# Optimization experiments

Measured on AMD Instinct MI355X. Metric: run time of the kernel, lower is better.

## Reference

```python
import jax, jax.numpy as jnp
import numpy as np

E = 512   # embed_size == hidden_size (required: step-0 'embed' is the init output of size hidden)
H = 512
A = 512   # attention dim
V = 20000
P = 196
B = 128
T = 24


def setup_inputs() -> dict:
    key = jax.random.key(0)
    ks = jax.random.split(key, 20)
    s = 0.02
    return {
        "features": jax.random.normal(ks[0], (B, P, E), jnp.float32),
        "captions": jax.random.randint(ks[1], (B, T), 0, V),
        "emb": jax.random.normal(ks[2], (V, E), jnp.float32) * s,
        "W_init_h": jax.random.normal(ks[3], (E, H), jnp.float32) * s,
        "b_init_h": jnp.zeros((H,), jnp.float32),
        "W_init_o": jax.random.normal(ks[4], (E, H), jnp.float32) * s,
        "b_init_o": jnp.zeros((H,), jnp.float32),
        "Wf": jax.random.normal(ks[5], (E, A), jnp.float32) * s,
        "bf": jnp.zeros((A,), jnp.float32),
        "Wh": jax.random.normal(ks[6], (H, A), jnp.float32) * s,
        "bh": jnp.zeros((A,), jnp.float32),
        "v_att": jax.random.normal(ks[7], (A,), jnp.float32) * s,
        "W_ih": jax.random.normal(ks[8], (3 * H, 2 * E), jnp.float32) * s,
        "W_hh": jax.random.normal(ks[9], (3 * H, H), jnp.float32) * s,
        "b_ih": jnp.zeros((3 * H,), jnp.float32),
        "b_hh": jnp.zeros((3 * H,), jnp.float32),
        "W_out": jax.random.normal(ks[10], (V, H), jnp.float32) * s,
        "b_out": jnp.zeros((V,), jnp.float32),
    }


def reference(features, emb, W_init_h, b_init_h, W_init_o, b_init_o,
              Wf, bf, Wh, bh, v_att, W_ih, W_hh, b_ih, b_hh,
              W_out, b_out, captions):
    # init_hidden_state
    avg = features.mean(axis=1)                          # [B,E]
    hidden0 = jnp.tanh(avg @ W_init_h + b_init_h)        # [B,H]
    output0 = jnp.tanh(avg @ W_init_o + b_init_o)        # [B,H]

    emb_caps = emb[captions]                             # [B,T,E]
    # teacher forcing: step 0 uses init output, step i>0 uses embeddings[:, i-1]
    embed_seq = jnp.concatenate([output0[:, None, :], emb_caps[:, :-1, :]], axis=1)
    xs = embed_seq.transpose(1, 0, 2)                    # [T,B,E]

    feat_proj = features @ Wf + bf                       # [B,P,A] (precompute attn key proj)

    def step(h, x_emb):
        # additive attention over pixels
        score = jnp.tanh(feat_proj + (h @ Wh + bh)[:, None, :]) @ v_att   # [B,P]
        alpha = jax.nn.softmax(score, axis=1)
        ctx = jnp.einsum('bp,bpe->be', alpha, features)                   # [B,E]
        x = jnp.concatenate([x_emb, ctx], axis=1)                         # [B,2E]
        # single-step GRU (PyTorch gate order r,z,n)
        gi = x @ W_ih.T + b_ih
        gh = h @ W_hh.T + b_hh
        gi_r, gi_z, gi_n = jnp.split(gi, 3, axis=1)
        gh_r, gh_z, gh_n = jnp.split(gh, 3, axis=1)
        r = jax.nn.sigmoid(gi_r + gh_r)
        z = jax.nn.sigmoid(gi_z + gh_z)
        n = jnp.tanh(gi_n + r * gh_n)
        h_new = (1.0 - z) * n + z * h
        pred = h_new @ W_out.T + b_out                                    # [B,V]
        return h_new, pred

    _, preds = jax.lax.scan(step, hidden0, xs)           # preds: [T,B,V]
    return preds.transpose(1, 0, 2)                      # [B,T,V]
```

## Files before the change

### kernel.cpp

```cpp
#include <hip/hip_runtime.h>

#define Bb 128
#define Tt 24
#define Ee 512
#define Hh 512
#define Aa 512
#define Vv 20000
#define Pp 196
#define TV (Tt*Vv)
#define NBLK 512
#define NTHR 256
#define GT (NBLK*NTHR)

typedef __attribute__((ext_vector_type(8))) short bfrag;
typedef __attribute__((ext_vector_type(4))) float f4;
typedef __attribute__((ext_vector_type(4))) unsigned short us4;
typedef __attribute__((ext_vector_type(2))) unsigned long long u64x2;

#define MFMA16(a,b,c) __builtin_amdgcn_mfma_f32_16x16x32_bf16(a,b,c,0,0,0)

__device__ __forceinline__ unsigned short f2bf(float f){
  unsigned int x = __builtin_bit_cast(unsigned int, f);
  x += 0x7fffu + ((x >> 16) & 1u);
  return (unsigned short)(x >> 16);
}
__device__ __forceinline__ float bfu2f(unsigned short u){
  unsigned int x = ((unsigned int)u) << 16;
  return __builtin_bit_cast(float, x);
}
#define LOG2E 1.442695041f
__device__ __forceinline__ float fexp2(float x){ return __builtin_amdgcn_exp2f(x); }
__device__ __forceinline__ float frcp (float x){ return __builtin_amdgcn_rcpf(x); }
__device__ __forceinline__ float tanh_f(float x){ return 1.0f - 2.0f*frcp(1.0f + fexp2((2.0f*LOG2E)*x)); }
__device__ __forceinline__ float sigm_f(float x){ return frcp(1.0f + fexp2(-LOG2E*x)); }

__device__ __forceinline__ unsigned long long scld8(const void* p){
  return __hip_atomic_load((const unsigned long long*)p, __ATOMIC_RELAXED, __HIP_MEMORY_SCOPE_AGENT);
}
__device__ __forceinline__ unsigned scld4(const unsigned* p){
  return __hip_atomic_load(p, __ATOMIC_RELAXED, __HIP_MEMORY_SCOPE_AGENT);
}
__device__ __forceinline__ bfrag scld_frag(const unsigned short* p){
  u64x2 v;
  v.x = scld8(p);
  v.y = scld8(p + 4);
  return __builtin_bit_cast(bfrag, v);
}
__device__ __forceinline__ void scst4(unsigned* p, unsigned v){
  __hip_atomic_store(p, v, __ATOMIC_RELAXED, __HIP_MEMORY_SCOPE_AGENT);
}
__device__ __forceinline__ void scstf(float* p, float v){
  __hip_atomic_store(p, v, __ATOMIC_RELAXED, __HIP_MEMORY_SCOPE_AGENT);
}

__device__ __forceinline__ void set_flag(unsigned* line, unsigned v){
  asm volatile("s_waitcnt vmcnt(0)" ::: "memory");
  __syncthreads();
  if(threadIdx.x == 0) scst4(line, v);
}
__device__ __forceinline__ void poll_flags(const unsigned* base, int n, unsigned tgt){
  int tid = threadIdx.x;
  for(;;){
    int ok = (tid < n) ? (scld4(base + tid*16) >= tgt) : 1;
    if(__syncthreads_count(ok) == NTHR) break;
    __builtin_amdgcn_s_sleep(2);
  }
  asm volatile("" ::: "memory");
}

__device__ __forceinline__ void gbar2(unsigned* sync, unsigned phase){
  __syncthreads();
  int tid = threadIdx.x, blk = blockIdx.x;
  if(tid == 0)
    (void)__hip_atomic_fetch_add(sync + (blk & 31)*16, 1u,
                                 __ATOMIC_RELEASE, __HIP_MEMORY_SCOPE_AGENT);
  if(blk == 0){
    for(;;){
      int ok = (tid < 32) ? (scld4(sync + tid*16) >= phase*16u) : 1;
      if(__syncthreads_count(ok) == NTHR) break;
      __builtin_amdgcn_s_sleep(2);
    }
    if(tid == 0) scst4(sync + 32*16, phase);
  }
  if(tid == 0){
    while(scld4(sync + 32*16) < phase) __builtin_amdgcn_s_sleep(2);
    (void)__hip_atomic_load(sync + 32*16, __ATOMIC_ACQUIRE, __HIP_MEMORY_SCOPE_AGENT);
  }
  __syncthreads();
}

__global__ void k_zero(unsigned* s){
  int i = blockIdx.x*256 + threadIdx.x;
  s[i] = 0u;
}

__device__ __forceinline__ void cast_loop(const float* __restrict__ s,
                                          unsigned short* __restrict__ d,
                                          int n4, int gtid){
  for(int i = gtid; i < n4; i += GT){
    float4 v = ((const float4*)s)[i];
    us4 o; o[0]=f2bf(v.x); o[1]=f2bf(v.y); o[2]=f2bf(v.z); o[3]=f2bf(v.w);
    ((us4*)d)[i] = o;
  }
}
__device__ __forceinline__ void tr_tile(const float* __restrict__ S,
                                        unsigned short* __restrict__ D,
                                        int it, int jt, int tid, float (*T)[33]){
  int er = tid>>3, c4 = (tid&7)*4;
  float4 v = *(const float4*)(S + (size_t)(jt*32+er)*512 + it*32 + c4);
  T[er][c4+0]=v.x; T[er][c4+1]=v.y; T[er][c4+2]=v.z; T[er][c4+3]=v.w;
  __syncthreads();
  us4 o;
  o[0]=f2bf(T[c4+0][er]); o[1]=f2bf(T[c4+1][er]);
  o[2]=f2bf(T[c4+2][er]); o[3]=f2bf(T[c4+3][er]);
  *(us4*)(D + (size_t)(it*32+er)*512 + jt*32 + c4) = o;
  __syncthreads();
}


__device__ void attention_task(int b, const float* __restrict__ hpr,
                               const unsigned short* __restrict__ fpb,
                               const unsigned short* __restrict__ featsB,
                               const float* __restrict__ vatt,
                               unsigned short* __restrict__ ctxb, char* SM)
{
  float* hp  = (float*)SM;
  float* vp  = hp + 512;
  float* sc  = vp + 512;
  float* red = sc + 200;
  int tid = threadIdx.x;
  {
    unsigned long long q = scld8(hpr + (size_t)b*Aa + tid*2);
    float2 hv = __builtin_bit_cast(float2, q);
    float2 vv = *(const float2*)(vatt + tid*2);
    int a0 = tid*2, a1 = tid*2+1;
    hp[((a0&31)<<4)+(a0>>5)] = hv.x;
    hp[((a1&31)<<4)+(a1>>5)] = hv.y;
    vp[((a0&31)<<4)+(a0>>5)] = vv.x;
    vp[((a1&31)<<4)+(a1>>5)] = vv.y;
  }
  __syncthreads();
  int grp = tid >> 4, gl = tid & 15;
  for(int pass=0; pass<13; pass++){
    int p = pass*16 + grp;
    float acc = 0.0f;
    if(p < Pp){
      const unsigned short* fr = fpb + ((size_t)b*Pp + p)*Aa + gl*32;
      #pragma unroll
      for(int j=0;j<32;j+=8){
        bfrag fv = *(const bfrag*)(fr + j);
        #pragma unroll
        for(int q=0;q<8;q++){
          int idx = ((j+q)<<4) + gl;
          float x = bfu2f((unsigned short)fv[q]) + hp[idx];
          acc += tanh_f(x) * vp[idx];
        }
      }
    }
    acc += __shfl_xor(acc, 1, 64);
    acc += __shfl_xor(acc, 2, 64);
    acc += __shfl_xor(acc, 4, 64);
    acc += __shfl_xor(acc, 8, 64);
    if(p < Pp && gl == 0) sc[p] = acc;
  }
  __syncthreads();
  if(tid < 64){
    float m = -1e30f;
    for(int i=0;i<4;i++){ int p = tid + i*64; if(p < Pp) m = fmaxf(m, sc[p]); }
    for(int off=1; off<64; off<<=1) m = fmaxf(m, __shfl_xor(m, off, 64));
    float s = 0.0f;
    for(int i=0;i<4;i++){ int p = tid + i*64; if(p < Pp) s += fexp2((sc[p]-m)*LOG2E); }
    for(int off=1; off<64; off<<=1) s += __shfl_xor(s, off, 64);
    if(tid == 0){ red[0] = m; red[1] = frcp(s); }
  }
  __syncthreads();
  float mx = red[0], rS = red[1];
  float al_t = 0.0f;
  if(tid < Pp) al_t = fexp2((sc[tid]-mx)*LOG2E) * rS;
  __syncthreads();
  if(tid < Pp) sc[tid] = al_t;
  __syncthreads();
  float c0 = 0.f, c1 = 0.f;
  const unsigned int* fb = (const unsigned int*)(featsB + (size_t)b*Pp*Ee);
  for(int p=0;p<Pp;p++){
    float al = sc[p];
    unsigned int u = fb[(size_t)p*256 + tid];
    unsigned int lo = (u & 0xffffu) << 16, hi = u & 0xffff0000u;
    c0 += al * __builtin_bit_cast(float, lo);
    c1 += al * __builtin_bit_cast(float, hi);
  }
  unsigned int cw = ((unsigned int)f2bf(c1) << 16) | (unsigned int)f2bf(c0);
  scst4((unsigned*)ctxb + (size_t)b*256 + tid, cw);
}

__device__ void gates_phaseA(int g, const unsigned short* __restrict__ hbs,
                             const unsigned short* __restrict__ aemb,
                             const unsigned short* __restrict__ WihB,
                             const unsigned short* __restrict__ WhhB,
                             f4 (&agh)[2][3], f4 (&agi)[2][3])
{
  int tid = threadIdx.x;
  int w = tid>>6, l = tid&63, l16 = l&15, lk = l>>4;
  int hs = g*16 + l16, m0 = w*32;
  #pragma unroll
  for(int mi=0;mi<2;mi++) for(int q=0;q<3;q++){ agh[mi][q]=(f4)(0.f); agi[mi][q]=(f4)(0.f); }
  bfrag ah0 = scld_frag(hbs + (size_t)(m0+l16)*Hh + lk*8);
  bfrag ah1 = scld_frag(hbs + (size_t)(m0+16+l16)*Hh + lk*8);
  for(int k0=0;k0<512;k0+=32){
    int koff = k0 + lk*8;
    bfrag nh0 = ah0, nh1 = ah1;
    if(k0+32 < 512){
      nh0 = scld_frag(hbs + (size_t)(m0+l16)*Hh + koff + 32);
      nh1 = scld_frag(hbs + (size_t)(m0+16+l16)*Hh + koff + 32);
    }
    bfrag ae0 = *(const bfrag*)(aemb + (size_t)(m0+l16)*Ee + koff);
    bfrag ae1 = *(const bfrag*)(aemb + (size_t)(m0+16+l16)*Ee + koff);
    #pragma unroll
    for(int q=0;q<3;q++){
      int j = q*512 + hs;
      bfrag bh_ = *(const bfrag*)(WhhB + (size_t)j*512  + koff);
      bfrag be  = *(const bfrag*)(WihB + (size_t)j*1024 + koff);
      agh[0][q] = MFMA16(ah0, bh_, agh[0][q]);
      agh[1][q] = MFMA16(ah1, bh_, agh[1][q]);
      agi[0][q] = MFMA16(ae0, be,  agi[0][q]);
      agi[1][q] = MFMA16(ae1, be,  agi[1][q]);
    }
    ah0 = nh0; ah1 = nh1;
  }
}

__device__ void gates_phaseB(int g, const unsigned short* __restrict__ ctxb,
                             const unsigned short* __restrict__ WihB,
                             const float* __restrict__ bih, const float* __restrict__ bhh,
                             const float* __restrict__ hf_cur, float* __restrict__ hf_nxt,
                             unsigned short* __restrict__ hb_nxt,
                             f4 (&agh)[2][3], f4 (&agi)[2][3], char* SM)
{
  unsigned short (*HB)[16] = (unsigned short(*)[16])SM;
  int tid = threadIdx.x;
  int w = tid>>6, l = tid&63, l16 = l&15, lk = l>>4;
  int hs = g*16 + l16, m0 = w*32;
  bfrag ac0 = scld_frag(ctxb + (size_t)(m0+l16)*Ee + lk*8);
  bfrag ac1 = scld_frag(ctxb + (size_t)(m0+16+l16)*Ee + lk*8);
  for(int k0=0;k0<512;k0+=32){
    int koff = k0 + lk*8;
    bfrag nc0 = ac0, nc1 = ac1;
    if(k0+32 < 512){
      nc0 = scld_frag(ctxb + (size_t)(m0+l16)*Ee + koff + 32);
      nc1 = scld_frag(ctxb + (size_t)(m0+16+l16)*Ee + koff + 32);
    }
    #pragma unroll
    for(int q=0;q<3;q++){
      int j = q*512 + hs;
      bfrag bc = *(const bfrag*)(WihB + (size_t)j*1024 + 512 + koff);
      agi[0][q] = MFMA16(ac0, bc, agi[0][q]);
      agi[1][q] = MFMA16(ac1, bc, agi[1][q]);
    }
    ac0 = nc0; ac1 = nc1;
  }
  float bir = bih[hs],      bhr = bhh[hs];
  float biz = bih[512+hs],  bhz = bhh[512+hs];
  float bin = bih[1024+hs], bhn = bhh[1024+hs];
  #pragma unroll
  for(int mi=0;mi<2;mi++){
    #pragma unroll
    for(int i=0;i<4;i++){
      int b = m0 + mi*16 + lk*4 + i;
      float r = sigm_f(agi[mi][0][i] + bir + agh[mi][0][i] + bhr);
      float z = sigm_f(agi[mi][1][i] + biz + agh[mi][1][i] + bhz);
      float n = tanh_f(agi[mi][2][i] + bin + r*(agh[mi][2][i] + bhn));
      float ho = hf_cur[(size_t)b*Hh + hs];
      float hn = (1.0f - z)*n + z*ho;
      hf_nxt[(size_t)b*Hh + hs] = hn;
      HB[b][l16] = f2bf(hn);
    }
  }
  __syncthreads();
  #pragma unroll
  for(int j2=0;j2<4;j2++){
    int wix = tid + j2*256;
    int bb = wix >> 3, pr = wix & 7;
    unsigned u = (unsigned)HB[bb][pr*2] | ((unsigned)HB[bb][pr*2+1] << 16);
    scst4((unsigned*)(hb_nxt + (size_t)bb*Hh + g*16) + pr, u);
  }
}

__device__ void hproj_task(int g, const unsigned short* __restrict__ hbsrc,
                           const unsigned short* __restrict__ WhT,
                           const float* __restrict__ bhv, float* __restrict__ hpr)
{
  int tid = threadIdx.x;
  int w = tid>>6, l = tid&63, l16 = l&15, lk = l>>4;
  int m0 = w*32;
  int a = g*16 + l16;
  f4 acc[2]; acc[0]=(f4)(0.0f); acc[1]=(f4)(0.0f);
  bfrag af0 = scld_frag(hbsrc + (size_t)(m0+l16)*Hh + lk*8);
  bfrag af1 = scld_frag(hbsrc + (size_t)(m0+16+l16)*Hh + lk*8);
  for(int k0=0;k0<512;k0+=32){
    int koff = k0 + lk*8;
    bfrag n0 = af0, n1 = af1;
    if(k0+32 < 512){
      n0 = scld_frag(hbsrc + (size_t)(m0+l16)*Hh + koff + 32);
      n1 = scld_frag(hbsrc + (size_t)(m0+16+l16)*Hh + koff + 32);
    }
    bfrag bq = *(const bfrag*)(WhT + (size_t)a*Hh + koff);
    acc[0] = MFMA16(af0, bq, acc[0]);
    acc[1] = MFMA16(af1, bq, acc[1]);
    af0 = n0; af1 = n1;
  }
  float bias = bhv[a];
  #pragma unroll
  for(int mi=0;mi<2;mi++)
    #pragma unroll
    for(int i=0;i<4;i++){
      int b = m0 + mi*16 + lk*4 + i;
      scstf(hpr + (size_t)b*Aa + a, acc[mi][i] + bias);
    }
}

__device__ void pred_task(int pt, int tw, const unsigned short* __restrict__ hb_cur,
                          const unsigned short* __restrict__ WoutB,
                          const float* __restrict__ bout, float* __restrict__ out,
                          char* SM)
{
  int tid = threadIdx.x;
  int vchunk = pt >> 1, mbase = (pt & 1)*64;
  for(int j=0;j<32;j++){
    int u = tid + j*256;
    int row = u >> 7, c8 = u & 127;
    unsigned long long q = scld8(hb_cur + (size_t)(mbase+row)*Hh + c8*4);
    int bo = (row<<10) + (c8<<3);
    bo ^= (row&7)<<4;
    *(unsigned long long*)(SM + bo) = q;
  }
  __syncthreads();
  int w = tid>>6, l = tid&63, l16 = l&15, lk = l>>4;
  int nb = vchunk*128 + w*32;
  f4 acc[4][2];
  #pragma unroll
  for(int mi=0;mi<4;mi++) for(int ni=0;ni<2;ni++) acc[mi][ni] = (f4)(0.0f);
  for(int k0=0;k0<512;k0+=32){
    int koff = k0 + lk*8;
    bfrag af[4], bq[2];
    #pragma unroll
    for(int mi=0;mi<4;mi++){
      int row = mi*16 + l16;
      int bo = (row<<10) + (koff<<1);
      bo ^= (row&7)<<4;
      af[mi] = *(const bfrag*)(SM + bo);
    }
    #pragma unroll
    for(int ni=0;ni<2;ni++){
      int v = nb + ni*16 + l16; if(v > Vv-1) v = Vv-1;
      bq[ni] = *(const bfrag*)(WoutB + (size_t)v*Hh + koff);
    }
    #pragma unroll
    for(int mi=0;mi<4;mi++)
      #pragma unroll
      for(int ni=0;ni<2;ni++)
        acc[mi][ni] = MFMA16(af[mi], bq[ni], acc[mi][ni]);
  }
  #pragma unroll
  for(int ni=0;ni<2;ni++){
    int v = nb + ni*16 + l16;
    if(v < Vv){
      float bias = bout[v];
      #pragma unroll
      for(int mi=0;mi<4;mi++){
        #pragma unroll
        for(int i=0;i<4;i++){
          int br = mbase + mi*16 + lk*4 + i;
          __builtin_nontemporal_store(acc[mi][ni][i] + bias,
              out + (size_t)br*TV + (size_t)tw*Vv + v);
        }
      }
    }
  }
  __syncthreads();
}

__global__ __launch_bounds__(NTHR, 2) void k_all(
    const float* feats, const int* caps, const float* emb,
    const float* Winh, const float* binh, const float* Wino, const float* bino,
    const float* Wf, const float* bfv, const float* Wh, const float* bhv,
    const float* vatt, const float* Wih, const float* Whh,
    const float* bih, const float* bhh, const float* Wout, const float* bout,
    float* out,
    float* hfR, unsigned short* hbR, float* hpr,
    unsigned short* ctxR, unsigned short* avgB, unsigned short* eseq,
    unsigned short* WfT, unsigned short* WhT,
    unsigned short* WinhT, unsigned short* WinoT,
    unsigned short* WihB, unsigned short* WhhB,
    unsigned short* fpb, unsigned short* featsB, unsigned short* WoutB,
    unsigned* sync)
{
  __shared__ char SMEM[65536];
  const int blk = blockIdx.x, tid = threadIdx.x;
  const int gtid = blk*NTHR + tid;
  unsigned* flagsA = sync + 33*16;
  unsigned* flagsH = sync + 161*16;
  unsigned* flagsP = sync + 193*16;
  float* h_f0 = hfR;
  unsigned short* h_b0 = hbR;

  cast_loop(Wih,  WihB,  (3*Hh*2*Ee)/4, gtid);
  cast_loop(Whh,  WhhB,  (3*Hh*Hh)/4,   gtid);
  cast_loop(Wout, WoutB, (Vv*Hh)/4,     gtid);
  cast_loop(feats,featsB,(Bb*Pp*Ee)/4,  gtid);
  for(int task = blk; task < 1024; task += NBLK){
    int z = task >> 8, rt = task & 255;
    int it = rt & 15, jt = rt >> 4;
    const float* S = (z==0)?Wf:(z==1)?Wh:(z==2)?Winh:Wino;
    unsigned short* D = (z==0)?WfT:(z==1)?WhT:(z==2)?WinhT:WinoT;
    tr_tile(S, D, it, jt, tid, (float(*)[33])SMEM);
  }
  if(blk < Bb){
    int b = blk;
    const float* fb = feats + (size_t)b*Pp*Ee;
    float a0=0.f, a1=0.f;
    for(int p=0;p<Pp;p++){
      float2 v = *(const float2*)(fb + (size_t)p*Ee + tid*2);
      a0 += v.x; a1 += v.y;
    }
    a0 *= (1.0f/Pp); a1 *= (1.0f/Pp);
    unsigned int pack = ((unsigned int)f2bf(a1)<<16) | (unsigned int)f2bf(a0);
    ((unsigned int*)avgB)[(size_t)b*256 + tid] = pack;
  }
  for(int task = blk; task < (Tt-1)*Bb; task += NBLK){
    int ts = task/Bb + 1, b = task%Bb;
    int cap = caps[b*Tt + (ts-1)];
    float2 v = *(const float2*)(emb + (size_t)cap*Ee + tid*2);
    unsigned int pack = ((unsigned int)f2bf(v.y)<<16) | (unsigned int)f2bf(v.x);
    ((unsigned int*)(eseq + ((size_t)ts*Bb + b)*Ee))[tid] = pack;
  }
  gbar2(sync, 1);

  for(int task = blk; task < 1584; task += NBLK){
    int w = tid>>6, l = tid&63, l16 = l&15, lk = l>>4;
    if(task < 1568){
      int bx = task % 196, by = task / 196;
      size_t m_base = (size_t)bx*128 + (w&1)*64;
      int nb = by*64 + (w>>1)*32;
      f4 acc[4][2];
      #pragma unroll
      for(int mi=0;mi<4;mi++) for(int ni=0;ni<2;ni++) acc[mi][ni] = (f4)(0.0f);
      for(int k0=0;k0<512;k0+=32){
        int koff = k0 + lk*8;
        bfrag af[4], bq[2];
        #pragma unroll
        for(int mi=0;mi<4;mi++) af[mi] = *(const bfrag*)(featsB + (m_base+mi*16+l16)*512 + koff);
        #pragma unroll
        for(int ni=0;ni<2;ni++) bq[ni] = *(const bfrag*)(WfT + (size_t)(nb+ni*16+l16)*512 + koff);
        #pragma unroll
        for(int mi=0;mi<4;mi++)
          #pragma unroll
          for(int ni=0;ni<2;ni++)
            acc[mi][ni] = MFMA16(af[mi], bq[ni], acc[mi][ni]);
      }
      #pragma unroll
      for(int ni=0;ni<2;ni++){
        int a = nb + ni*16 + l16;
        float bias = bfv[a];
        #pragma unroll
        for(int mi=0;mi<4;mi++){
          size_t r = m_base + mi*16 + lk*4;
          #pragma unroll
          for(int i=0;i<4;i++)
            fpb[(r+i)*512 + a] = f2bf(acc[mi][ni][i] + bias);
        }
      }
    } else {
      int idx = task - 1568;
      int y = idx >> 3, xb = idx & 7;
      int m0 = (w&1)*64, nb = xb*64 + (w>>1)*32;
      const unsigned short* Wt = y ? WinoT : WinhT;
      const float* bias = y ? bino : binh;
      f4 acc[4][2];
      #pragma unroll
      for(int mi=0;mi<4;mi++) for(int ni=0;ni<2;ni++) acc[mi][ni] = (f4)(0.0f);
      for(int k0=0;k0<512;k0+=32){
        int koff = k0 + lk*8;
        bfrag af[4], bq[2];
        #pragma unroll
        for(int mi=0;mi<4;mi++) af[mi] = *(const bfrag*)(avgB + (size_t)(m0+mi*16+l16)*512 + koff);
        #pragma unroll
        for(int ni=0;ni<2;ni++) bq[ni] = *(const bfrag*)(Wt + (size_t)(nb+ni*16+l16)*512 + koff);
        #pragma unroll
        for(int mi=0;mi<4;mi++)
          #pragma unroll
          for(int ni=0;ni<2;ni++)
            acc[mi][ni] = MFMA16(af[mi], bq[ni], acc[mi][ni]);
      }
      #pragma unroll
      for(int ni=0;ni<2;ni++){
        int n = nb + ni*16 + l16;
        float bv = bias[n];
        #pragma unroll
        for(int mi=0;mi<4;mi++){
          int bb = m0 + mi*16 + lk*4;
          #pragma unroll
          for(int i=0;i<4;i++){
            float val = tanh_f(acc[mi][ni][i] + bv);
            if(y==0){ h_f0[(size_t)(bb+i)*Hh + n] = val; h_b0[(size_t)(bb+i)*Hh + n] = f2bf(val); }
            else    { eseq[(size_t)(bb+i)*Ee + n] = f2bf(val); }
          }
        }
      }
    }
  }
  gbar2(sync, 2);

  int xcd = blk & 7, slot = blk >> 3;

  if(slot < 16){
    int b = xcd*16 + slot;
    for(int t=0; t<Tt; t++){
      poll_flags(flagsP, 32, (unsigned)(t+1));
      attention_task(b, hpr + (size_t)(t&1)*Bb*Aa, fpb, featsB, vatt,
                     ctxR + (size_t)(t&1)*Bb*Ee, SMEM);
      set_flag(flagsA + b*16, (unsigned)(t+1));
    }
  } else if(slot < 20){
    int g = xcd*4 + (slot-16);
    f4 agh[2][3], agi[2][3];
    hproj_task(g, hbR, WhT, bhv, hpr);
    set_flag(flagsP + g*16, 1u);
    gates_phaseA(g, hbR, eseq, WihB, WhhB, agh, agi);
    for(int t=0; t<Tt; t++){
      poll_flags(flagsA, 128, (unsigned)(t+1));
      gates_phaseB(g, ctxR + (size_t)(t&1)*Bb*Ee, WihB, bih, bhh,
                   hfR + (size_t)(t&1)*Bb*Hh, hfR + (size_t)((t+1)&1)*Bb*Hh,
                   hbR + (size_t)(t+1)*Bb*Hh, agh, agi, SMEM);
      set_flag(flagsH + g*16, (unsigned)(t+1));
      if(t+1 < Tt){
        poll_flags(flagsH, 32, (unsigned)(t+1));
        hproj_task(g, hbR + (size_t)(t+1)*Bb*Hh, WhT, bhv,
                   hpr + (size_t)((t+1)&1)*Bb*Aa);
        set_flag(flagsP + g*16, (unsigned)(t+2));
        gates_phaseA(g, hbR + (size_t)(t+1)*Bb*Hh, eseq + (size_t)(t+1)*Bb*Ee,
                     WihB, WhhB, agh, agi);
      }
    }
  } else if(slot < 60){
    int pt = xcd*40 + (slot-20);
    if(pt < 314){
      for(int t=1; t<=Tt; t++){
        poll_flags(flagsH, 32, (unsigned)t);
        pred_task(pt, t-1, hbR + (size_t)t*Bb*Hh, WoutB, bout, out, SMEM);
      }
    }
  }
}

extern "C" void kernel_launch(void* const* d_in, const int* in_sizes, int n_in,
                              void* d_out, int out_size, void* d_ws, size_t ws_size,
                              hipStream_t stream)
{
  const float* feats = (const float*)d_in[0];
  const int*   caps  = (const int*)d_in[1];
  const float* emb   = (const float*)d_in[2];
  const float* Winh  = (const float*)d_in[3];
  const float* binh  = (const float*)d_in[4];
  const float* Wino  = (const float*)d_in[5];
  const float* bino  = (const float*)d_in[6];
  const float* Wf    = (const float*)d_in[7];
  const float* bfv   = (const float*)d_in[8];
  const float* Wh    = (const float*)d_in[9];
  const float* bhv   = (const float*)d_in[10];
  const float* vatt  = (const float*)d_in[11];
  const float* Wih   = (const float*)d_in[12];
  const float* Whh   = (const float*)d_in[13];
  const float* bih   = (const float*)d_in[14];
  const float* bhh   = (const float*)d_in[15];
  const float* Wout  = (const float*)d_in[16];
  const float* bout  = (const float*)d_in[17];
  float* out = (float*)d_out;

  char* ws = (char*)d_ws;
  size_t off = 0;
  auto alloc = [&](size_t bytes){
    off = (off + 255) & ~(size_t)255;
    void* p = ws + off; off += bytes; return p;
  };
  unsigned* syncp = (unsigned*)alloc(16384);
  float* hfR = (float*)alloc((size_t)2*Bb*Hh*4);
  unsigned short* hbR = (unsigned short*)alloc((size_t)(Tt+1)*Bb*Hh*2);
  float* hpr = (float*)alloc((size_t)2*Bb*Aa*4);
  unsigned short* ctxR  = (unsigned short*)alloc((size_t)2*Bb*Ee*2);
  unsigned short* avgB  = (unsigned short*)alloc((size_t)Bb*Ee*2);
  unsigned short* eseq  = (unsigned short*)alloc((size_t)Tt*Bb*Ee*2);
  unsigned short* WfT   = (unsigned short*)alloc((size_t)Ee*Aa*2);
  unsigned short* WhT   = (unsigned short*)alloc((size_t)Hh*Aa*2);
  unsigned short* WinhT = (unsigned short*)alloc((size_t)Ee*Hh*2);
  unsigned short* WinoT = (unsigned short*)alloc((size_t)Ee*Hh*2);
  unsigned short* WihB  = (unsigned short*)alloc((size_t)3*Hh*2*Ee*2);
  unsigned short* WhhB  = (unsigned short*)alloc((size_t)3*Hh*Hh*2);
  unsigned short* fpb   = (unsigned short*)alloc((size_t)Bb*Pp*Aa*2);
  unsigned short* featsB= (unsigned short*)alloc((size_t)Bb*Pp*Ee*2);
  unsigned short* WoutB = (unsigned short*)alloc((size_t)Vv*Hh*2);
  if(ws_size < off) return;

  k_zero<<<16, 256, 0, stream>>>(syncp);
  k_all<<<NBLK, NTHR, 0, stream>>>(
      feats, caps, emb, Winh, binh, Wino, bino, Wf, bfv, Wh, bhv, vatt,
      Wih, Whh, bih, bhh, Wout, bout, out,
      hfR, hbR, hpr, ctxR, avgB, eseq,
      WfT, WhT, WinhT, WinoT, WihB, WhhB, fpb, featsB, WoutB, syncp);
}
```

Baseline: 1.639 ms.

## Fuse h-projection into attention and tile GRU gates by row-group to localize sync

Removes the separate h@Wh projection task. Each attention block now computes its own batch row's projection from the bf16 hidden state with scalar FMAs. GRU gate work is re-tiled into 8 row-groups by 8 column-groups (64 blocks), each staging its 16 rows of h and ctx into swizzled LDS, so blocks wait only on flags from their own row group instead of global all-to-all flags. Prediction blocks poll one per-XCD aggregated flag, and ctx is quad-buffered. The cost is redundant per-row projection compute in attention and more blocks devoted to gates.

```diff
diff --git a/kernel.cpp b/kernel.cpp
--- a/kernel.cpp
+++ b/kernel.cpp
@@ -15,7 +15,6 @@
 typedef __attribute__((ext_vector_type(8))) short bfrag;
 typedef __attribute__((ext_vector_type(4))) float f4;
 typedef __attribute__((ext_vector_type(4))) unsigned short us4;
-typedef __attribute__((ext_vector_type(2))) unsigned long long u64x2;
 
 #define MFMA16(a,b,c) __builtin_amdgcn_mfma_f32_16x16x32_bf16(a,b,c,0,0,0)
 
@@ -40,16 +39,7 @@
 __device__ __forceinline__ unsigned scld4(const unsigned* p){
   return __hip_atomic_load(p, __ATOMIC_RELAXED, __HIP_MEMORY_SCOPE_AGENT);
 }
-__device__ __forceinline__ bfrag scld_frag(const unsigned short* p){
-  u64x2 v;
-  v.x = scld8(p);
-  v.y = scld8(p + 4);
-  return __builtin_bit_cast(bfrag, v);
-}
 __device__ __forceinline__ void scst4(unsigned* p, unsigned v){
-  __hip_atomic_store(p, v, __ATOMIC_RELAXED, __HIP_MEMORY_SCOPE_AGENT);
-}
-__device__ __forceinline__ void scstf(float* p, float v){
   __hip_atomic_store(p, v, __ATOMIC_RELAXED, __HIP_MEMORY_SCOPE_AGENT);
 }
 
@@ -63,7 +53,7 @@
   for(;;){
     int ok = (tid < n) ? (scld4(base + tid*16) >= tgt) : 1;
     if(__syncthreads_count(ok) == NTHR) break;
-    __builtin_amdgcn_s_sleep(2);
+    __builtin_amdgcn_s_sleep(4);
   }
   asm volatile("" ::: "memory");
 }
@@ -117,27 +107,55 @@
   __syncthreads();
 }
 
-
-__device__ void attention_task(int b, const float* __restrict__ hpr,
+__device__ __forceinline__ void stage16(char* dstSM, const unsigned short* src, int R0){
+  int tid = threadIdx.x;
+  #pragma unroll
+  for(int j=0;j<8;j++){
+    int u = tid + j*256;
+    int row = u >> 7, c8 = u & 127;
+    unsigned long long q = scld8(src + (size_t)(R0+row)*Hh + c8*4);
+    int bo = (row<<10) + (c8<<3);
+    bo ^= (row&7)<<4;
+    *(unsigned long long*)(dstSM + bo) = q;
+  }
+}
+
+
+__device__ void attention_task(int b, const unsigned short* __restrict__ hbU_t,
+                               const unsigned short* __restrict__ WhT, const float* __restrict__ bhv,
                                const unsigned short* __restrict__ fpb,
                                const unsigned short* __restrict__ featsB,
                                const float* __restrict__ vatt,
-                               unsigned short* __restrict__ ctxb, char* SM)
+                               unsigned short* __restrict__ ctx_t, char* SM)
 {
-  float* hp  = (float*)SM;
+  float* h_s = (float*)SM;
+  float* hp  = h_s + 512;
   float* vp  = hp + 512;
   float* sc  = vp + 512;
   float* red = sc + 200;
   int tid = threadIdx.x;
-  {
-    unsigned long long q = scld8(hpr + (size_t)b*Aa + tid*2);
-    float2 hv = __builtin_bit_cast(float2, q);
-    float2 vv = *(const float2*)(vatt + tid*2);
-    int a0 = tid*2, a1 = tid*2+1;
-    hp[((a0&31)<<4)+(a0>>5)] = hv.x;
-    hp[((a1&31)<<4)+(a1>>5)] = hv.y;
+  if(tid < 128){
+    unsigned long long q8 = scld8(hbU_t + (size_t)b*Hh + tid*4);
+    h_s[tid*4+0] = bfu2f((unsigned short)(q8));
+    h_s[tid*4+1] = bfu2f((unsigned short)(q8>>16));
+    h_s[tid*4+2] = bfu2f((unsigned short)(q8>>32));
+    h_s[tid*4+3] = bfu2f((unsigned short)(q8>>48));
+  }
+  { float2 vv = *(const float2*)(vatt + tid*2);
+    int a0=tid*2, a1=a0+1;
     vp[((a0&31)<<4)+(a0>>5)] = vv.x;
-    vp[((a1&31)<<4)+(a1>>5)] = vv.y;
+    vp[((a1&31)<<4)+(a1>>5)] = vv.y; }
+  __syncthreads();
+  for(int rep=0;rep<2;rep++){
+    int a = tid + rep*256;
+    float s = bhv[a];
+    const unsigned short* wr = WhT + (size_t)a*Hh;
+    for(int k=0;k<Hh;k+=8){
+      bfrag wv = *(const bfrag*)(wr + k);
+      #pragma unroll
+      for(int q=0;q<8;q++) s += h_s[k+q] * bfu2f((unsigned short)wv[q]);
+    }
+    hp[((a&31)<<4)+(a>>5)] = s;
   }
   __syncthreads();
   int grp = tid >> 4, gl = tid & 15;
@@ -190,132 +208,80 @@
     c1 += al * __builtin_bit_cast(float, hi);
   }
   unsigned int cw = ((unsigned int)f2bf(c1) << 16) | (unsigned int)f2bf(c0);
-  scst4((unsigned*)ctxb + (size_t)b*256 + tid, cw);
-}
-
-__device__ void gates_phaseA(int g, const unsigned short* __restrict__ hbs,
-                             const unsigned short* __restrict__ aemb,
+  scst4((unsigned*)ctx_t + (size_t)b*256 + tid, cw);
+}
+
+__device__ void gates_phaseA(int R0, int HC0, const unsigned short* __restrict__ eseqT,
                              const unsigned short* __restrict__ WihB,
                              const unsigned short* __restrict__ WhhB,
-                             f4 (&agh)[2][3], f4 (&agi)[2][3])
+                             const char* SMh, f4 (&agh)[3], f4 (&agi)[3])
 {
   int tid = threadIdx.x;
   int w = tid>>6, l = tid&63, l16 = l&15, lk = l>>4;
-  int hs = g*16 + l16, m0 = w*32;
+  int hcol = HC0 + w*16 + l16;
   #pragma unroll
-  for(int mi=0;mi<2;mi++) for(int q=0;q<3;q++){ agh[mi][q]=(f4)(0.f); agi[mi][q]=(f4)(0.f); }
-  bfrag ah0 = scld_frag(hbs + (size_t)(m0+l16)*Hh + lk*8);
-  bfrag ah1 = scld_frag(hbs + (size_t)(m0+16+l16)*Hh + lk*8);
+  for(int q=0;q<3;q++){ agh[q]=(f4)(0.f); agi[q]=(f4)(0.f); }
   for(int k0=0;k0<512;k0+=32){
     int koff = k0 + lk*8;
-    bfrag nh0 = ah0, nh1 = ah1;
-    if(k0+32 < 512){
-      nh0 = scld_frag(hbs + (size_t)(m0+l16)*Hh + koff + 32);
-      nh1 = scld_frag(hbs + (size_t)(m0+16+l16)*Hh + koff + 32);
-    }
-    bfrag ae0 = *(const bfrag*)(aemb + (size_t)(m0+l16)*Ee + koff);
-    bfrag ae1 = *(const bfrag*)(aemb + (size_t)(m0+16+l16)*Ee + koff);
+    int bo = (l16<<10) + (koff<<1); bo ^= (l16&7)<<4;
+    bfrag ah = *(const bfrag*)(SMh + bo);
+    bfrag ae = *(const bfrag*)(eseqT + (size_t)(R0+l16)*Ee + koff);
     #pragma unroll
     for(int q=0;q<3;q++){
-      int j = q*512 + hs;
+      int j = q*512 + hcol;
       bfrag bh_ = *(const bfrag*)(WhhB + (size_t)j*512  + koff);
       bfrag be  = *(const bfrag*)(WihB + (size_t)j*1024 + koff);
-      agh[0][q] = MFMA16(ah0, bh_, agh[0][q]);
-      agh[1][q] = MFMA16(ah1, bh_, agh[1][q]);
-      agi[0][q] = MFMA16(ae0, be,  agi[0][q]);
-      agi[1][q] = MFMA16(ae1, be,  agi[1][q]);
-    }
-    ah0 = nh0; ah1 = nh1;
-  }
-}
-
-__device__ void gates_phaseB(int g, const unsigned short* __restrict__ ctxb,
+      agh[q] = MFMA16(ah, bh_, agh[q]);
+      agi[q] = MFMA16(ae, be,  agi[q]);
+    }
+  }
+}
+
+__device__ void gates_phaseB(int R0, int HC0, const char* SMc,
                              const unsigned short* __restrict__ WihB,
                              const float* __restrict__ bih, const float* __restrict__ bhh,
                              const float* __restrict__ hf_cur, float* __restrict__ hf_nxt,
-                             unsigned short* __restrict__ hb_nxt,
-                             f4 (&agh)[2][3], f4 (&agi)[2][3], char* SM)
-{
-  unsigned short (*HB)[16] = (unsigned short(*)[16])SM;
-  int tid = threadIdx.x;
-  int w = tid>>6, l = tid&63, l16 = l&15, lk = l>>4;
-  int hs = g*16 + l16, m0 = w*32;
-  bfrag ac0 = scld_frag(ctxb + (size_t)(m0+l16)*Ee + lk*8);
-  bfrag ac1 = scld_frag(ctxb + (size_t)(m0+16+l16)*Ee + lk*8);
-  for(int k0=0;k0<512;k0+=32){
-    int koff = k0 + lk*8;
-    bfrag nc0 = ac0, nc1 = ac1;
-    if(k0+32 < 512){
-      nc0 = scld_frag(ctxb + (size_t)(m0+l16)*Ee + koff + 32);
-      nc1 = scld_frag(ctxb + (size_t)(m0+16+l16)*Ee + koff + 32);
-    }
-    #pragma unroll
-    for(int q=0;q<3;q++){
-      int j = q*512 + hs;
-      bfrag bc = *(const bfrag*)(WihB + (size_t)j*1024 + 512 + koff);
-      agi[0][q] = MFMA16(ac0, bc, agi[0][q]);
-      agi[1][q] = MFMA16(ac1, bc, agi[1][q]);
-    }
-    ac0 = nc0; ac1 = nc1;
-  }
-  float bir = bih[hs],      bhr = bhh[hs];
-  float biz = bih[512+hs],  bhz = bhh[512+hs];
-  float bin = bih[1024+hs], bhn = bhh[1024+hs];
-  #pragma unroll
-  for(int mi=0;mi<2;mi++){
-    #pragma unroll
-    for(int i=0;i<4;i++){
-      int b = m0 + mi*16 + lk*4 + i;
-      float r = sigm_f(agi[mi][0][i] + bir + agh[mi][0][i] + bhr);
-      float z = sigm_f(agi[mi][1][i] + biz + agh[mi][1][i] + bhz);
-      float n = tanh_f(agi[mi][2][i] + bin + r*(agh[mi][2][i] + bhn));
-      float ho = hf_cur[(size_t)b*Hh + hs];
-      float hn = (1.0f - z)*n + z*ho;
-      hf_nxt[(size_t)b*Hh + hs] = hn;
-      HB[b][l16] = f2bf(hn);
-    }
-  }
-  __syncthreads();
-  #pragma unroll
-  for(int j2=0;j2<4;j2++){
-    int wix = tid + j2*256;
-    int bb = wix >> 3, pr = wix & 7;
-    unsigned u = (unsigned)HB[bb][pr*2] | ((unsigned)HB[bb][pr*2+1] << 16);
-    scst4((unsigned*)(hb_nxt + (size_t)bb*Hh + g*16) + pr, u);
-  }
-}
-
-__device__ void hproj_task(int g, const unsigned short* __restrict__ hbsrc,
-                           const unsigned short* __restrict__ WhT,
-                           const float* __restrict__ bhv, float* __restrict__ hpr)
+                             unsigned short* __restrict__ hbU_nxt,
+                             f4 (&agh)[3], f4 (&agi)[3], char* SM_HB)
 {
   int tid = threadIdx.x;
   int w = tid>>6, l = tid&63, l16 = l&15, lk = l>>4;
-  int m0 = w*32;
-  int a = g*16 + l16;
-  f4 acc[2]; acc[0]=(f4)(0.0f); acc[1]=(f4)(0.0f);
-  bfrag af0 = scld_frag(hbsrc + (size_t)(m0+l16)*Hh + lk*8);
-  bfrag af1 = scld_frag(hbsrc + (size_t)(m0+16+l16)*Hh + lk*8);
+  int hcol = HC0 + w*16 + l16;
   for(int k0=0;k0<512;k0+=32){
     int koff = k0 + lk*8;
-    bfrag n0 = af0, n1 = af1;
-    if(k0+32 < 512){
-      n0 = scld_frag(hbsrc + (size_t)(m0+l16)*Hh + koff + 32);
-      n1 = scld_frag(hbsrc + (size_t)(m0+16+l16)*Hh + koff + 32);
-    }
-    bfrag bq = *(const bfrag*)(WhT + (size_t)a*Hh + koff);
-    acc[0] = MFMA16(af0, bq, acc[0]);
-    acc[1] = MFMA16(af1, bq, acc[1]);
-    af0 = n0; af1 = n1;
-  }
-  float bias = bhv[a];
+    int bo = (l16<<10) + (koff<<1); bo ^= (l16&7)<<4;
+    bfrag ac = *(const bfrag*)(SMc + bo);
+    #pragma unroll
+    for(int q=0;q<3;q++){
+      int j = q*512 + hcol;
+      bfrag bc = *(const bfrag*)(WihB + (size_t)j*1024 + 512 + koff);
+      agi[q] = MFMA16(ac, bc, agi[q]);
+    }
+  }
+  float bir = bih[hcol],      bhr = bhh[hcol];
+  float biz = bih[512+hcol],  bhz = bhh[512+hcol];
+  float bin = bih[1024+hcol], bhn = bhh[1024+hcol];
+  unsigned short (*HB)[64] = (unsigned short(*)[64])SM_HB;
   #pragma unroll
-  for(int mi=0;mi<2;mi++)
-    #pragma unroll
-    for(int i=0;i<4;i++){
-      int b = m0 + mi*16 + lk*4 + i;
-      scstf(hpr + (size_t)b*Aa + a, acc[mi][i] + bias);
-    }
+  for(int i=0;i<4;i++){
+    int row = lk*4 + i;
+    int b = R0 + row;
+    float r_ = sigm_f(agi[0][i] + bir + agh[0][i] + bhr);
+    float z_ = sigm_f(agi[1][i] + biz + agh[1][i] + bhz);
+    float n_ = tanh_f(agi[2][i] + bin + r_*(agh[2][i] + bhn));
+    float ho = hf_cur[(size_t)b*Hh + hcol];
+    float hn = (1.0f - z_)*n_ + z_*ho;
+    hf_nxt[(size_t)b*Hh + hcol] = hn;
+    HB[row][w*16 + l16] = f2bf(hn);
+  }
+  __syncthreads();
+  #pragma unroll
+  for(int j=0;j<2;j++){
+    int widx = tid + j*256;
+    int row = widx >> 5, pr = widx & 31;
+    unsigned uu = (unsigned)HB[row][pr*2] | ((unsigned)HB[row][pr*2+1] << 16);
+    scst4((unsigned*)(hbU_nxt + (size_t)(R0+row)*Hh + HC0) + pr, uu);
+  }
 }
 
 __device__ void pred_task(int pt, int tw, const unsigned short* __restrict__ hb_cur,
@@ -386,7 +352,7 @@
     const float* vatt, const float* Wih, const float* Whh,
     const float* bih, const float* bhh, const float* Wout, const float* bout,
     float* out,
-    float* hfR, unsigned short* hbR, float* hpr,
+    float* hfR, unsigned short* hbU,
     unsigned short* ctxR, unsigned short* avgB, unsigned short* eseq,
     unsigned short* WfT, unsigned short* WhT,
     unsigned short* WinhT, unsigned short* WinoT,
@@ -397,11 +363,11 @@
   __shared__ char SMEM[65536];
   const int blk = blockIdx.x, tid = threadIdx.x;
   const int gtid = blk*NTHR + tid;
-  unsigned* flagsA = sync + 33*16;
-  unsigned* flagsH = sync + 161*16;
-  unsigned* flagsP = sync + 193*16;
+  unsigned* flagsA = sync + 40*16;
+  unsigned* flagsG = sync + 168*16;
+  unsigned* aggP   = sync + 240*16;
   float* h_f0 = hfR;
-  unsigned short* h_b0 = hbR;
+  unsigned short* h_b0 = hbU;
 
   cast_loop(Wih,  WihB,  (3*Hh*2*Ee)/4, gtid);
   cast_loop(Whh,  WhhB,  (3*Hh*Hh)/4,   gtid);
@@ -513,40 +479,52 @@
   int xcd = blk & 7, slot = blk >> 3;
 
   if(slot < 16){
-    int b = xcd*16 + slot;
+    int b = slot*8 + xcd;
+    int rg = b >> 4;
     for(int t=0; t<Tt; t++){
-      poll_flags(flagsP, 32, (unsigned)(t+1));
-      attention_task(b, hpr + (size_t)(t&1)*Bb*Aa, fpb, featsB, vatt,
-                     ctxR + (size_t)(t&1)*Bb*Ee, SMEM);
+      if(t > 0) poll_flags(flagsG + rg*8*16, 8, (unsigned)t);
+      attention_task(b, hbU + (size_t)t*Bb*Hh, WhT, bhv, fpb, featsB, vatt,
+                     ctxR + (size_t)(t&3)*Bb*Ee, SMEM);
       set_flag(flagsA + b*16, (unsigned)(t+1));
     }
-  } else if(slot < 20){
-    int g = xcd*4 + (slot-16);
-    f4 agh[2][3], agi[2][3];
-    hproj_task(g, hbR, WhT, bhv, hpr);
-    set_flag(flagsP + g*16, 1u);
-    gates_phaseA(g, hbR, eseq, WihB, WhhB, agh, agi);
+  } else if(slot < 24){
+    int r = slot - 16, c = xcd;
+    int R0 = r*16, HC0 = c*64;
+    char* SMh = SMEM;
+    char* SMc = SMEM + 16384;
+    char* SMB = SMEM + 32768;
+    f4 agh[3], agi[3];
+    stage16(SMh, hbU, R0);
+    __syncthreads();
+    gates_phaseA(R0, HC0, eseq, WihB, WhhB, SMh, agh, agi);
     for(int t=0; t<Tt; t++){
-      poll_flags(flagsA, 128, (unsigned)(t+1));
-      gates_phaseB(g, ctxR + (size_t)(t&1)*Bb*Ee, WihB, bih, bhh,
+      poll_flags(flagsA + R0*16, 16, (unsigned)(t+1));
+      stage16(SMc, ctxR + (size_t)(t&3)*Bb*Ee, R0);
+      __syncthreads();
+      gates_phaseB(R0, HC0, SMc, WihB, bih, bhh,
                    hfR + (size_t)(t&1)*Bb*Hh, hfR + (size_t)((t+1)&1)*Bb*Hh,
-                   hbR + (size_t)(t+1)*Bb*Hh, agh, agi, SMEM);
-      set_flag(flagsH + g*16, (unsigned)(t+1));
+                   hbU + (size_t)(t+1)*Bb*Hh, agh, agi, SMB);
+      set_flag(flagsG + (r*8+c)*16, (unsigned)(t+1));
       if(t+1 < Tt){
-        poll_flags(flagsH, 32, (unsigned)(t+1));
-        hproj_task(g, hbR + (size_t)(t+1)*Bb*Hh, WhT, bhv,
-                   hpr + (size_t)((t+1)&1)*Bb*Aa);
-        set_flag(flagsP + g*16, (unsigned)(t+2));
-        gates_phaseA(g, hbR + (size_t)(t+1)*Bb*Hh, eseq + (size_t)(t+1)*Bb*Ee,
-                     WihB, WhhB, agh, agi);
-      }
-    }
-  } else if(slot < 60){
-    int pt = xcd*40 + (slot-20);
-    if(pt < 314){
+        poll_flags(flagsG + r*8*16, 8, (unsigned)(t+1));
+        stage16(SMh, hbU + (size_t)(t+1)*Bb*Hh, R0);
+        __syncthreads();
+        gates_phaseA(R0, HC0, eseq + (size_t)(t+1)*Bb*Ee, WihB, WhhB, SMh, agh, agi);
+      }
+    }
+  } else {
+    int ps = slot - 24;
+    int pt = xcd*40 + ps;
+    if(ps == 0){
       for(int t=1; t<=Tt; t++){
-        poll_flags(flagsH, 32, (unsigned)t);
-        pred_task(pt, t-1, hbR + (size_t)t*Bb*Hh, WoutB, bout, out, SMEM);
+        poll_flags(flagsG, 64, (unsigned)t);
+        if(tid == 0) scst4(aggP + xcd*16, (unsigned)t);
+        pred_task(pt, t-1, hbU + (size_t)t*Bb*Hh, WoutB, bout, out, SMEM);
+      }
+    } else if(pt < 314){
+      for(int t=1; t<=Tt; t++){
+        poll_flags(aggP + xcd*16, 1, (unsigned)t);
+        pred_task(pt, t-1, hbU + (size_t)t*Bb*Hh, WoutB, bout, out, SMEM);
       }
     }
   }
@@ -584,9 +562,8 @@
   };
   unsigned* syncp = (unsigned*)alloc(16384);
   float* hfR = (float*)alloc((size_t)2*Bb*Hh*4);
-  unsigned short* hbR = (unsigned short*)alloc((size_t)(Tt+1)*Bb*Hh*2);
-  float* hpr = (float*)alloc((size_t)2*Bb*Aa*4);
-  unsigned short* ctxR  = (unsigned short*)alloc((size_t)2*Bb*Ee*2);
+  unsigned short* hbU = (unsigned short*)alloc((size_t)(Tt+1)*Bb*Hh*2);
+  unsigned short* ctxR  = (unsigned short*)alloc((size_t)4*Bb*Ee*2);
   unsigned short* avgB  = (unsigned short*)alloc((size_t)Bb*Ee*2);
   unsigned short* eseq  = (unsigned short*)alloc((size_t)Tt*Bb*Ee*2);
   unsigned short* WfT   = (unsigned short*)alloc((size_t)Ee*Aa*2);
@@ -604,6 +581,6 @@
   k_all<<<NBLK, NTHR, 0, stream>>>(
       feats, caps, emb, Winh, binh, Wino, bino, Wf, bfv, Wh, bhv, vatt,
       Wih, Whh, bih, bhh, Wout, bout, out,
-      hfR, hbR, hpr, ctxR, avgB, eseq,
+      hfR, hbU, ctxR, avgB, eseq,
       WfT, WhT, WinhT, WinoT, WihB, WhhB, fpb, featsB, WoutB, syncp);
 }
```

Result: slower. 1.676 ms (+2.3%).
